# Performance work log

Measured on AMD Instinct MI355X. Metric: run time of the kernel, lower is better.

The kernel has to match this reference:

```python
import jax, jax.numpy as jnp
import numpy as np


def setup_inputs() -> dict:
    key = jax.random.key(0)
    ks = jax.random.split(key, 7)
    B, S, IN, OUT = 4, 2048, 4096, 4096
    R_DEC, R_TR = 1024, 64
    return {
        "x": jax.random.normal(ks[0], (B, S, IN), dtype=jnp.float32),
        "siva_u_t": jax.random.normal(ks[1], (OUT, R_TR), dtype=jnp.float32) * 0.02,
        "siva_u_d": jax.random.normal(ks[2], (OUT, R_DEC - R_TR), dtype=jnp.float32) * 0.02,
        "siva_s": jax.random.uniform(ks[3], (R_DEC,), dtype=jnp.float32),
        "siva_v_t": jax.random.normal(ks[4], (R_TR, IN), dtype=jnp.float32) * 0.02,
        "siva_v_d": jax.random.normal(ks[5], (R_DEC - R_TR, IN), dtype=jnp.float32) * 0.02,
        "bias": jax.random.normal(ks[6], (OUT,), dtype=jnp.float32) * 0.02,
    }


def reference(x, siva_u_t, siva_u_d, siva_s, siva_v_t, siva_v_d, bias):
    # Faithful to torch: weight = (cat(U_t, U_d, dim=1) * S) @ cat(V_t, V_d, dim=0)
    siva_u = jnp.concatenate((siva_u_t, siva_u_d), axis=1)   # [out, r]
    siva_v = jnp.concatenate((siva_v_t, siva_v_d), axis=0)   # [r, in]
    weight = (siva_u * siva_s) @ siva_v                       # [out, in]
    # F.linear: x @ weight.T + bias
    return jnp.einsum("bsi,oi->bso", x, weight) + bias
```

## Files before the change

### kernel.cpp

```cpp
#include <hip/hip_runtime.h>
#include <cstdint>


#define BM 128
#define BN 128
#define BK 32

typedef __bf16 bf16x8 __attribute__((ext_vector_type(8)));
typedef float f32x4 __attribute__((ext_vector_type(4)));

__device__ __forceinline__ unsigned short f32_to_bf16(float f) {
    union { float f; uint32_t u; } v; v.f = f;
    uint32_t u = v.u;
    u += 0x7FFF + ((u >> 16) & 1);
    return (unsigned short)(u >> 16);
}

__global__ void cast_f32_bf16(const float* __restrict__ src,
                              unsigned short* __restrict__ dst, int n4) {
    int i = blockIdx.x * blockDim.x + threadIdx.x;
    if (i >= n4) return;
    float4 v = ((const float4*)src)[i];
    ushort4 o;
    o.x = f32_to_bf16(v.x); o.y = f32_to_bf16(v.y);
    o.z = f32_to_bf16(v.z); o.w = f32_to_bf16(v.w);
    ((ushort4*)dst)[i] = o;
}

__global__ void build_u(const float* __restrict__ u_t, const float* __restrict__ u_d,
                        const float* __restrict__ s, unsigned short* __restrict__ ub,
                        int n4) {
    int i = blockIdx.x * blockDim.x + threadIdx.x;
    if (i >= n4) return;
    int e = i * 4;
    int o = e >> 10;
    int r = e & 1023;
    float4 u;
    if (r < 64) u = *(const float4*)(u_t + (size_t)o * 64 + r);
    else        u = *(const float4*)(u_d + (size_t)o * 960 + (r - 64));
    float4 sv = *(const float4*)(s + r);
    ushort4 w;
    w.x = f32_to_bf16(u.x * sv.x);
    w.y = f32_to_bf16(u.y * sv.y);
    w.z = f32_to_bf16(u.z * sv.z);
    w.w = f32_to_bf16(u.w * sv.w);
    ((ushort4*)ub)[i] = w;
}

__device__ __forceinline__ void stage16(const unsigned short* g, unsigned short* l) {
    __builtin_amdgcn_global_load_lds(
        (const __attribute__((address_space(1))) uint32_t*)g,
        (__attribute__((address_space(3))) uint32_t*)l, 16, 0, 0);
}

template <int MODE>
__global__ __launch_bounds__(256)
void gemm_nt(const unsigned short* __restrict__ A, const unsigned short* __restrict__ B,
             int K, int N,
             unsigned short* __restrict__ Cb, float* __restrict__ Cf,
             const float* __restrict__ bias) {
    __shared__ unsigned short ldsA[BM * BK];
    __shared__ unsigned short ldsB[BN * BK];

    const int tid  = threadIdx.x;
    const int wave = tid >> 6, lane = tid & 63;
    const int wm = wave >> 1, wn = wave & 1;
    const int q = lane >> 4, l16 = lane & 15;
    const int m0 = blockIdx.y * BM, n0 = blockIdx.x * BN;

    f32x4 acc[4][4] = {};

    const int rowc = tid >> 2;
    const int colc = (tid & 3) << 3;
    const unsigned short* gA0 = A + (size_t)(m0 + rowc) * K + colc;
    const unsigned short* gA1 = A + (size_t)(m0 + rowc + 64) * K + colc;
    const unsigned short* gB0 = B + (size_t)(n0 + rowc) * K + colc;
    const unsigned short* gB1 = B + (size_t)(n0 + rowc + 64) * K + colc;
    unsigned short* lA0 = ldsA + tid * 8;
    unsigned short* lA1 = ldsA + (tid + 256) * 8;
    unsigned short* lB0 = ldsB + tid * 8;
    unsigned short* lB1 = ldsB + (tid + 256) * 8;

    const int nKT = K / BK;
    for (int kt = 0; kt < nKT; ++kt) {
        const int k0 = kt * BK;
        stage16(gA0 + k0, lA0);
        stage16(gA1 + k0, lA1);
        stage16(gB0 + k0, lB0);
        stage16(gB1 + k0, lB1);
        asm volatile("s_waitcnt vmcnt(0)" ::: "memory");
        __syncthreads();

        bf16x8 af[4], bfr[4];
#pragma unroll
        for (int t = 0; t < 4; ++t) {
            af[t]  = *(const bf16x8*)(ldsA + (wm * 64 + t * 16 + l16) * BK + q * 8);
            bfr[t] = *(const bf16x8*)(ldsB + (wn * 64 + t * 16 + l16) * BK + q * 8);
        }
#pragma unroll
        for (int mt = 0; mt < 4; ++mt)
#pragma unroll
            for (int nt = 0; nt < 4; ++nt)
                acc[mt][nt] = __builtin_amdgcn_mfma_f32_16x16x32_bf16(
                    af[mt], bfr[nt], acc[mt][nt], 0, 0, 0);
        __syncthreads();
    }

#pragma unroll
    for (int mt = 0; mt < 4; ++mt) {
#pragma unroll
        for (int nt = 0; nt < 4; ++nt) {
            const int col = n0 + wn * 64 + nt * 16 + l16;
            const int rbase = m0 + wm * 64 + mt * 16 + q * 4;
            float bv = (MODE == 1) ? bias[col] : 0.0f;
#pragma unroll
            for (int i = 0; i < 4; ++i) {
                const int row = rbase + i;
                float v = acc[mt][nt][i];
                if (MODE == 0)
                    Cb[(size_t)row * N + col] = f32_to_bf16(v);
                else
                    Cf[(size_t)row * N + col] = v + bv;
            }
        }
    }
}

extern "C" void kernel_launch(void* const* d_in, const int* in_sizes, int n_in,
                              void* d_out, int out_size, void* d_ws, size_t ws_size,
                              hipStream_t stream) {
    const float* x    = (const float*)d_in[0];
    const float* u_t  = (const float*)d_in[1];
    const float* u_d  = (const float*)d_in[2];
    const float* s    = (const float*)d_in[3];
    const float* v_t  = (const float*)d_in[4];
    const float* v_d  = (const float*)d_in[5];
    const float* bias = (const float*)d_in[6];
    float* out = (float*)d_out;

    const int M = 8192, IN = 4096, R = 1024, OUT = 4096;

    char* ws = (char*)d_ws;
    unsigned short* xb = (unsigned short*)ws;
    unsigned short* Vb = (unsigned short*)(ws + (size_t)(64 << 20));
    unsigned short* Ub = (unsigned short*)(ws + (size_t)(72 << 20));
    unsigned short* Y  = (unsigned short*)(ws + (size_t)(80 << 20));

    {
        int n4 = M * IN / 4;
        cast_f32_bf16<<<(n4 + 255) / 256, 256, 0, stream>>>(x, xb, n4);
    }
    {
        int n4 = 64 * IN / 4;
        cast_f32_bf16<<<(n4 + 255) / 256, 256, 0, stream>>>(v_t, Vb, n4);
    }
    {
        int n4 = 960 * IN / 4;
        cast_f32_bf16<<<(n4 + 255) / 256, 256, 0, stream>>>(v_d, Vb + 64 * IN, n4);
    }
    {
        int n4 = OUT * R / 4;
        build_u<<<(n4 + 255) / 256, 256, 0, stream>>>(u_t, u_d, s, Ub, n4);
    }

    gemm_nt<0><<<dim3(R / BN, M / BM), 256, 0, stream>>>(xb, Vb, IN, R, Y, nullptr, nullptr);
    gemm_nt<1><<<dim3(OUT / BN, M / BM), 256, 0, stream>>>(Y, Ub, R, OUT, nullptr, out, bias);
}
```

Before: 444.4 us.

## Fuse x cast into first GEMM with split-K and swizzled tile order

Removes the standalone fp32-to-bf16 cast of x by loading fp32 activations in the first GEMM and converting them in registers before storing to LDS. The first GEMM is split along K into two halves writing fp32 partials, which a new reduce kernel sums and casts to bf16. Both GEMMs remap block indices so groups of M-tiles share B tiles in L2. This trades the cast pass for extra partial-sum traffic and synchronous register-path loads of A.

```diff
diff --git a/kernel.cpp b/kernel.cpp
--- a/kernel.cpp
+++ b/kernel.cpp
@@ -8,6 +8,7 @@
 
 typedef __bf16 bf16x8 __attribute__((ext_vector_type(8)));
 typedef float f32x4 __attribute__((ext_vector_type(4)));
+typedef unsigned short u16x8 __attribute__((ext_vector_type(8)));
 
 __device__ __forceinline__ unsigned short f32_to_bf16(float f) {
     union { float f; uint32_t u; } v; v.f = f;
@@ -53,12 +54,18 @@
         (__attribute__((address_space(3))) uint32_t*)l, 16, 0, 0);
 }
 
-template <int MODE>
+__device__ __forceinline__ void cvt_store8(unsigned short* l, float4 a, float4 b) {
+    u16x8 w;
+    w[0] = f32_to_bf16(a.x); w[1] = f32_to_bf16(a.y);
+    w[2] = f32_to_bf16(a.z); w[3] = f32_to_bf16(a.w);
+    w[4] = f32_to_bf16(b.x); w[5] = f32_to_bf16(b.y);
+    w[6] = f32_to_bf16(b.z); w[7] = f32_to_bf16(b.w);
+    *(u16x8*)l = w;
+}
+
 __global__ __launch_bounds__(256)
-void gemm_nt(const unsigned short* __restrict__ A, const unsigned short* __restrict__ B,
-             int K, int N,
-             unsigned short* __restrict__ Cb, float* __restrict__ Cf,
-             const float* __restrict__ bias) {
+void gemm_a_fused(const float* __restrict__ X, const unsigned short* __restrict__ V,
+                  float* __restrict__ Yp) {
     __shared__ unsigned short ldsA[BM * BK];
     __shared__ unsigned short ldsB[BN * BK];
 
@@ -66,23 +73,116 @@
     const int wave = tid >> 6, lane = tid & 63;
     const int wm = wave >> 1, wn = wave & 1;
     const int q = lane >> 4, l16 = lane & 15;
-    const int m0 = blockIdx.y * BM, n0 = blockIdx.x * BN;
+
+    const int b = blockIdx.x + (blockIdx.y << 3);
+    const int c = b & 7;
+    const int t = b >> 3;
+    const int tx = t & 7;
+    const int ty = ((t >> 3) << 3) + c;
+    const int m0 = ty * BM, n0 = tx * BN;
+    const int kbase = blockIdx.z * 2048;
 
     f32x4 acc[4][4] = {};
 
     const int rowc = tid >> 2;
     const int colc = (tid & 3) << 3;
-    const unsigned short* gA0 = A + (size_t)(m0 + rowc) * K + colc;
-    const unsigned short* gA1 = A + (size_t)(m0 + rowc + 64) * K + colc;
-    const unsigned short* gB0 = B + (size_t)(n0 + rowc) * K + colc;
-    const unsigned short* gB1 = B + (size_t)(n0 + rowc + 64) * K + colc;
+    const float* gX0 = X + (size_t)(m0 + rowc) * 4096 + kbase + colc;
+    const float* gX1 = gX0 + (size_t)64 * 4096;
+    const unsigned short* gB0 = V + (size_t)(n0 + rowc) * 4096 + kbase + colc;
+    const unsigned short* gB1 = gB0 + (size_t)64 * 4096;
     unsigned short* lA0 = ldsA + tid * 8;
     unsigned short* lA1 = ldsA + (tid + 256) * 8;
     unsigned short* lB0 = ldsB + tid * 8;
     unsigned short* lB1 = ldsB + (tid + 256) * 8;
 
-    const int nKT = K / BK;
-    for (int kt = 0; kt < nKT; ++kt) {
+    for (int kt = 0; kt < 64; ++kt) {
+        const int k0 = kt * BK;
+        stage16(gB0 + k0, lB0);
+        stage16(gB1 + k0, lB1);
+        float4 a0 = *(const float4*)(gX0 + k0);
+        float4 a1 = *(const float4*)(gX0 + k0 + 4);
+        float4 a2 = *(const float4*)(gX1 + k0);
+        float4 a3 = *(const float4*)(gX1 + k0 + 4);
+        cvt_store8(lA0, a0, a1);
+        cvt_store8(lA1, a2, a3);
+        asm volatile("s_waitcnt vmcnt(0)" ::: "memory");
+        __syncthreads();
+
+        bf16x8 af[4], bfr[4];
+#pragma unroll
+        for (int i = 0; i < 4; ++i) {
+            af[i]  = *(const bf16x8*)(ldsA + (wm * 64 + i * 16 + l16) * BK + q * 8);
+            bfr[i] = *(const bf16x8*)(ldsB + (wn * 64 + i * 16 + l16) * BK + q * 8);
+        }
+#pragma unroll
+        for (int mt = 0; mt < 4; ++mt)
+#pragma unroll
+            for (int nt = 0; nt < 4; ++nt)
+                acc[mt][nt] = __builtin_amdgcn_mfma_f32_16x16x32_bf16(
+                    af[mt], bfr[nt], acc[mt][nt], 0, 0, 0);
+        __syncthreads();
+    }
+
+    float* out = Yp + (size_t)blockIdx.z * 8192 * 1024;
+#pragma unroll
+    for (int mt = 0; mt < 4; ++mt)
+#pragma unroll
+        for (int nt = 0; nt < 4; ++nt) {
+            const int col = n0 + wn * 64 + nt * 16 + l16;
+            const int rbase = m0 + wm * 64 + mt * 16 + q * 4;
+#pragma unroll
+            for (int i = 0; i < 4; ++i)
+                out[(size_t)(rbase + i) * 1024 + col] = acc[mt][nt][i];
+        }
+}
+
+__global__ void reduce_y(const float* __restrict__ p0, const float* __restrict__ p1,
+                         unsigned short* __restrict__ y, int n4) {
+    int i = blockIdx.x * blockDim.x + threadIdx.x;
+    if (i >= n4) return;
+    float4 a = ((const float4*)p0)[i];
+    float4 b = ((const float4*)p1)[i];
+    ushort4 w;
+    w.x = f32_to_bf16(a.x + b.x);
+    w.y = f32_to_bf16(a.y + b.y);
+    w.z = f32_to_bf16(a.z + b.z);
+    w.w = f32_to_bf16(a.w + b.w);
+    ((ushort4*)y)[i] = w;
+}
+
+__global__ __launch_bounds__(256)
+void gemm_b(const unsigned short* __restrict__ A, const unsigned short* __restrict__ B,
+            float* __restrict__ C, const float* __restrict__ bias) {
+    __shared__ unsigned short ldsA[BM * BK];
+    __shared__ unsigned short ldsB[BN * BK];
+
+    const int tid  = threadIdx.x;
+    const int wave = tid >> 6, lane = tid & 63;
+    const int wm = wave >> 1, wn = wave & 1;
+    const int q = lane >> 4, l16 = lane & 15;
+
+    const int b = blockIdx.x + (blockIdx.y << 5);
+    const int c = b & 7;
+    const int t = b >> 3;
+    const int tx = t & 31;
+    const int ty = ((t >> 5) << 3) + c;
+    const int m0 = ty * BM, n0 = tx * BN;
+
+    const int K = 1024, N = 4096;
+    f32x4 acc[4][4] = {};
+
+    const int rowc = tid >> 2;
+    const int colc = (tid & 3) << 3;
+    const unsigned short* gA0 = A + (size_t)(m0 + rowc) * K + colc;
+    const unsigned short* gA1 = gA0 + (size_t)64 * K;
+    const unsigned short* gB0 = B + (size_t)(n0 + rowc) * K + colc;
+    const unsigned short* gB1 = gB0 + (size_t)64 * K;
+    unsigned short* lA0 = ldsA + tid * 8;
+    unsigned short* lA1 = ldsA + (tid + 256) * 8;
+    unsigned short* lB0 = ldsB + tid * 8;
+    unsigned short* lB1 = ldsB + (tid + 256) * 8;
+
+    for (int kt = 0; kt < K / BK; ++kt) {
         const int k0 = kt * BK;
         stage16(gA0 + k0, lA0);
         stage16(gA1 + k0, lA1);
@@ -93,9 +193,9 @@
 
         bf16x8 af[4], bfr[4];
 #pragma unroll
-        for (int t = 0; t < 4; ++t) {
-            af[t]  = *(const bf16x8*)(ldsA + (wm * 64 + t * 16 + l16) * BK + q * 8);
-            bfr[t] = *(const bf16x8*)(ldsB + (wn * 64 + t * 16 + l16) * BK + q * 8);
+        for (int i = 0; i < 4; ++i) {
+            af[i]  = *(const bf16x8*)(ldsA + (wm * 64 + i * 16 + l16) * BK + q * 8);
+            bfr[i] = *(const bf16x8*)(ldsB + (wn * 64 + i * 16 + l16) * BK + q * 8);
         }
 #pragma unroll
         for (int mt = 0; mt < 4; ++mt)
@@ -107,23 +207,16 @@
     }
 
 #pragma unroll
-    for (int mt = 0; mt < 4; ++mt) {
+    for (int mt = 0; mt < 4; ++mt)
 #pragma unroll
         for (int nt = 0; nt < 4; ++nt) {
             const int col = n0 + wn * 64 + nt * 16 + l16;
             const int rbase = m0 + wm * 64 + mt * 16 + q * 4;
-            float bv = (MODE == 1) ? bias[col] : 0.0f;
-#pragma unroll
-            for (int i = 0; i < 4; ++i) {
-                const int row = rbase + i;
-                float v = acc[mt][nt][i];
-                if (MODE == 0)
-                    Cb[(size_t)row * N + col] = f32_to_bf16(v);
-                else
-                    Cf[(size_t)row * N + col] = v + bv;
-            }
-        }
-    }
+            const float bv = bias[col];
+#pragma unroll
+            for (int i = 0; i < 4; ++i)
+                C[(size_t)(rbase + i) * N + col] = acc[mt][nt][i] + bv;
+        }
 }
 
 extern "C" void kernel_launch(void* const* d_in, const int* in_sizes, int n_in,
@@ -141,15 +234,11 @@
     const int M = 8192, IN = 4096, R = 1024, OUT = 4096;
 
     char* ws = (char*)d_ws;
-    unsigned short* xb = (unsigned short*)ws;
+    float*          Yp = (float*)ws;
     unsigned short* Vb = (unsigned short*)(ws + (size_t)(64 << 20));
     unsigned short* Ub = (unsigned short*)(ws + (size_t)(72 << 20));
-    unsigned short* Y  = (unsigned short*)(ws + (size_t)(80 << 20));
-
-    {
-        int n4 = M * IN / 4;
-        cast_f32_bf16<<<(n4 + 255) / 256, 256, 0, stream>>>(x, xb, n4);
-    }
+    unsigned short* Yb = (unsigned short*)(ws + (size_t)(80 << 20));
+
     {
         int n4 = 64 * IN / 4;
         cast_f32_bf16<<<(n4 + 255) / 256, 256, 0, stream>>>(v_t, Vb, n4);
@@ -163,6 +252,10 @@
         build_u<<<(n4 + 255) / 256, 256, 0, stream>>>(u_t, u_d, s, Ub, n4);
     }
 
-    gemm_nt<0><<<dim3(R / BN, M / BM), 256, 0, stream>>>(xb, Vb, IN, R, Y, nullptr, nullptr);
-    gemm_nt<1><<<dim3(OUT / BN, M / BM), 256, 0, stream>>>(Y, Ub, R, OUT, nullptr, out, bias);
-}
+    gemm_a_fused<<<dim3(R / BN, M / BM, 2), 256, 0, stream>>>(x, Vb, Yp);
+    {
+        int n4 = M * R / 4;
+        reduce_y<<<(n4 + 255) / 256, 256, 0, stream>>>(Yp, Yp + (size_t)M * R, Yb, n4);
+    }
+    gemm_b<<<dim3(OUT / BN, M / BM), 256, 0, stream>>>(Yb, Ub, out, bias);
+}
```

Result: slower. 455.5 us (+2.5%).
